# Kernel tuning notes

Hardware: AMD Instinct MI355X
Metric: run time of the kernel (lower is better)

Reference implementation:

```python
import jax, jax.numpy as jnp
import numpy as np

N, E, T = 50000, 800000, 3
FIN, H, D, FE = 256, 4, 64, 64
NEG_SLOPE = 0.2


def setup_inputs() -> dict:
    key = jax.random.key(0)
    ks = jax.random.split(key, 10)
    x = jax.random.normal(ks[0], (N, FIN), dtype=jnp.float32)
    edge_src = jax.random.randint(ks[1], (E,), 0, N, dtype=jnp.int32)
    edge_dst = jax.random.randint(ks[2], (E,), 0, N, dtype=jnp.int32)
    edge_type = jax.random.randint(ks[3], (E,), 0, T, dtype=jnp.int32)
    s = 1.0 / np.sqrt(FIN)
    W = jax.random.normal(ks[4], (FIN, H * D), dtype=jnp.float32) * s
    edge_emb = jax.random.normal(ks[5], (T, FE), dtype=jnp.float32)
    W_e = jax.random.normal(ks[6], (FE, H * FE), dtype=jnp.float32) * (1.0 / np.sqrt(FE))
    attn_l = jax.random.normal(ks[7], (H, D), dtype=jnp.float32) * (1.0 / np.sqrt(D))
    attn_r = jax.random.normal(ks[8], (H, D), dtype=jnp.float32) * (1.0 / np.sqrt(D))
    attn_e = jax.random.normal(ks[9], (H, FE), dtype=jnp.float32) * (1.0 / np.sqrt(FE))
    return {"x": x, "edge_src": edge_src, "edge_dst": edge_dst,
            "edge_type": edge_type, "W": W, "edge_emb": edge_emb,
            "W_e": W_e, "attn_l": attn_l, "attn_r": attn_r, "attn_e": attn_e}


def reference(x, edge_src, edge_dst, edge_type, W, edge_emb, W_e, attn_l, attn_r, attn_e):
    # node projection: [N, H, D]
    feat = (x @ W).reshape(N, H, D)
    # per-node, per-head attention scalars
    el = jnp.einsum('nhd,hd->nh', feat, attn_l)  # [N, H]
    er = jnp.einsum('nhd,hd->nh', feat, attn_r)  # [N, H]
    # per-edge-type attention scalar: edge_emb[t] @ W_e -> [T, H, FE]
    e_feat = (edge_emb @ W_e).reshape(T, H, FE)
    ee = jnp.einsum('the,he->th', e_feat, attn_e)  # [T, H]
    # per-edge logits, leaky-relu
    logits = jax.nn.leaky_relu(el[edge_src] + er[edge_dst] + ee[edge_type], NEG_SLOPE)  # [E, H]
    # edge softmax over incoming edges of each dst node (all etypes together)
    seg_max = jax.ops.segment_max(logits, edge_dst, num_segments=N)  # [N, H]
    seg_max = jnp.where(jnp.isfinite(seg_max), seg_max, 0.0)
    expl = jnp.exp(logits - seg_max[edge_dst])  # [E, H]
    seg_sum = jax.ops.segment_sum(expl, edge_dst, num_segments=N)  # [N, H]
    a = expl / seg_sum[edge_dst]  # [E, H]
    # weighted scatter-sum aggregation: sum over incoming edges
    msg = feat[edge_src] * a[:, :, None]  # [E, H, D]
    out = jax.ops.segment_sum(msg, edge_dst, num_segments=N)  # [N, H, D]
    return out, a
```

## Files before the change

kernel.cpp:

```cpp
#include <hip/hip_runtime.h>
#include <hip/hip_bf16.h>
#include <math.h>

#define N_NODES 50000
#define E_EDGES 800000
#define T_TYPES 3
#define MAXDEG 64
#define NEG_SLOPE 0.2f
#define GEMM_BLOCKS 391

typedef __attribute__((ext_vector_type(8))) short short8;
typedef __attribute__((ext_vector_type(4))) float f32x4;

__device__ inline short f2bf(float f) {
    __hip_bfloat16 h = __float2bfloat16(f);
    union { __hip_bfloat16 b; short s; } u;
    u.b = h;
    return u.s;
}
__device__ inline float bf2f(short s) {
    union { unsigned u; float f; } v;
    v.u = ((unsigned)(unsigned short)s) << 16;
    return v.f;
}

__global__ void k_prep(const float* __restrict__ W, short* __restrict__ Wt,
                       const float* __restrict__ edge_emb, const float* __restrict__ W_e,
                       const float* __restrict__ attn_e, float* __restrict__ ee,
                       unsigned* __restrict__ deg) {
    int b = blockIdx.x;
    if (b < 256) {
        int n = b, k = threadIdx.x;
        Wt[n * 256 + k] = f2bf(W[k * 256 + n]);
    } else if (b < 256 + T_TYPES) {
        int t = b - 256;
        int j = threadIdx.x;
        int h = j >> 6;
        float ae = attn_e[j];
        float v = 0.f;
        #pragma unroll
        for (int k = 0; k < 64; ++k) v += edge_emb[t * 64 + k] * W_e[k * 256 + j];
        v *= ae;
        #pragma unroll
        for (int o = 32; o; o >>= 1) v += __shfl_xor(v, o, 64);
        if ((j & 63) == 0) ee[t * 4 + h] = v;
    } else {
        int i = (b - 256 - T_TYPES) * 256 + threadIdx.x;
        if (i < N_NODES) deg[i] = 0u;
    }
}

__global__ __launch_bounds__(512) void k_gs(const float* __restrict__ x, const short* __restrict__ Wt,
                                            const float* __restrict__ attn_l, const float* __restrict__ attn_r,
                                            short* __restrict__ featb, float* __restrict__ el,
                                            float* __restrict__ er,
                                            const int* __restrict__ esrc, const int* __restrict__ edst,
                                            const int* __restrict__ etype, unsigned* __restrict__ deg,
                                            unsigned* __restrict__ A) {
    __shared__ short a_lds[2][128 * 40];
    if (blockIdx.x >= GEMM_BLOCKS) {
        int e = (blockIdx.x - GEMM_BLOCKS) * 512 + threadIdx.x;
        if (e < E_EDGES) {
            int s = esrc[e], d = edst[e], t = etype[e];
            unsigned rank = atomicAdd(&deg[d], 1u);
            if (rank < MAXDEG)
                A[d * MAXDEG + rank] = (unsigned)s | ((unsigned)t << 16);
        }
        return;
    }

    const int tid = threadIdx.x;
    const int wid = tid >> 6;
    const int lane = tid & 63;
    const int wr = wid >> 2;
    const int wc = wid & 3;
    const int l15 = lane & 15;
    const int lq = lane >> 4;
    const int m0 = blockIdx.x * 128;

    f32x4 acc[4][4];
    #pragma unroll
    for (int mf = 0; mf < 4; ++mf)
        #pragma unroll
        for (int nf = 0; nf < 4; ++nf)
            acc[mf][nf] = (f32x4){0.f, 0.f, 0.f, 0.f};

    const int sr = tid >> 2;
    const int sc = (tid & 3) * 8;
    int gm = m0 + sr;
    if (gm >= N_NODES) gm = N_NODES - 1;
    const float* xrow = &x[(size_t)gm * 256];

    {
        float4 v0 = *reinterpret_cast<const float4*>(&xrow[sc]);
        float4 v1 = *reinterpret_cast<const float4*>(&xrow[sc + 4]);
        short8 s;
        s[0] = f2bf(v0.x); s[1] = f2bf(v0.y); s[2] = f2bf(v0.z); s[3] = f2bf(v0.w);
        s[4] = f2bf(v1.x); s[5] = f2bf(v1.y); s[6] = f2bf(v1.z); s[7] = f2bf(v1.w);
        *reinterpret_cast<short8*>(&a_lds[0][sr * 40 + sc]) = s;
    }
    __syncthreads();

    #pragma unroll
    for (int k0 = 0; k0 < 256; k0 += 32) {
        const int cur = (k0 >> 5) & 1;
        const bool hasNext = (k0 + 32) < 256;
        float4 v0, v1;
        if (hasNext) {
            v0 = *reinterpret_cast<const float4*>(&xrow[k0 + 32 + sc]);
            v1 = *reinterpret_cast<const float4*>(&xrow[k0 + 32 + sc + 4]);
        }
        short8 av[4], bv[4];
        #pragma unroll
        for (int mf = 0; mf < 4; ++mf)
            av[mf] = *reinterpret_cast<const short8*>(&a_lds[cur][(wr * 64 + mf * 16 + l15) * 40 + lq * 8]);
        #pragma unroll
        for (int nf = 0; nf < 4; ++nf) {
            int n = wc * 64 + nf * 16 + l15;
            bv[nf] = *reinterpret_cast<const short8*>(&Wt[(size_t)n * 256 + k0 + lq * 8]);
        }
        if (hasNext) {
            short8 s;
            s[0] = f2bf(v0.x); s[1] = f2bf(v0.y); s[2] = f2bf(v0.z); s[3] = f2bf(v0.w);
            s[4] = f2bf(v1.x); s[5] = f2bf(v1.y); s[6] = f2bf(v1.z); s[7] = f2bf(v1.w);
            *reinterpret_cast<short8*>(&a_lds[cur ^ 1][sr * 40 + sc]) = s;
        }
        #pragma unroll
        for (int mf = 0; mf < 4; ++mf)
            #pragma unroll
            for (int nf = 0; nf < 4; ++nf)
                acc[mf][nf] = __builtin_amdgcn_mfma_f32_16x16x32_bf16(av[mf], bv[nf], acc[mf][nf], 0, 0, 0);
        __syncthreads();
    }

    float al[4], ar[4];
    #pragma unroll
    for (int nf = 0; nf < 4; ++nf) {
        al[nf] = attn_l[wc * 64 + nf * 16 + l15];
        ar[nf] = attn_r[wc * 64 + nf * 16 + l15];
    }
    #pragma unroll
    for (int mf = 0; mf < 4; ++mf) {
        #pragma unroll
        for (int i = 0; i < 4; ++i) {
            int m = m0 + wr * 64 + mf * 16 + lq * 4 + i;
            bool ok = m < N_NODES;
            float pl = 0.f, pr = 0.f;
            #pragma unroll
            for (int nf = 0; nf < 4; ++nf) {
                float v = acc[mf][nf][i];
                if (ok) featb[(size_t)m * 256 + wc * 64 + nf * 16 + l15] = f2bf(v);
                pl += v * al[nf];
                pr += v * ar[nf];
            }
            #pragma unroll
            for (int o = 1; o < 16; o <<= 1) {
                pl += __shfl_xor(pl, o, 64);
                pr += __shfl_xor(pr, o, 64);
            }
            if (ok && l15 == 0) {
                el[m * 4 + wc] = pl;
                er[m * 4 + wc] = pr;
            }
        }
    }
}

__global__ __launch_bounds__(256) void k_agg(const unsigned* __restrict__ deg, const unsigned* __restrict__ A,
                                             const float* __restrict__ el, const float* __restrict__ er,
                                             const float* __restrict__ ee, const short* __restrict__ featb,
                                             float* __restrict__ out, float* __restrict__ invp) {
    const int wave = threadIdx.x >> 6;
    const int lane = threadIdx.x & 63;
    const int n = blockIdx.x * 4 + wave;
    if (n >= N_NODES) return;
    const int half = lane >> 5;
    const int l32 = lane & 31;
    const int h = l32 >> 3;
    unsigned cnt = deg[n];
    if (cnt > MAXDEG) cnt = MAXDEG;
    const unsigned base = (unsigned)n * MAXDEG;

    const float ern = er[n * 4 + h];
    const float ee0 = ee[h], ee1 = ee[4 + h], ee2 = ee[8 + h];

    float s0 = 0.f, s1 = 0.f;
    float a0[8], a1[8];
    #pragma unroll
    for (int j = 0; j < 8; ++j) { a0[j] = 0.f; a1[j] = 0.f; }
    {
        unsigned i = half;
        for (; i + 2 < cnt; i += 4) {
            unsigned p0 = A[base + i];
            unsigned p1 = A[base + i + 2];
            unsigned src0 = p0 & 0xFFFFu, t0 = p0 >> 16;
            unsigned src1 = p1 & 0xFFFFu, t1 = p1 >> 16;
            float el0 = el[src0 * 4 + h];
            float el1 = el[src1 * 4 + h];
            short8 f0 = *reinterpret_cast<const short8*>(&featb[(size_t)src0 * 256 + l32 * 8]);
            short8 f1 = *reinterpret_cast<const short8*>(&featb[(size_t)src1 * 256 + l32 * 8]);
            float z0 = (el0 + ern) + (t0 == 0 ? ee0 : (t0 == 1 ? ee1 : ee2));
            float z1 = (el1 + ern) + (t1 == 0 ? ee0 : (t1 == 1 ? ee1 : ee2));
            z0 = z0 > 0.f ? z0 : NEG_SLOPE * z0;
            z1 = z1 > 0.f ? z1 : NEG_SLOPE * z1;
            float w0 = __expf(z0);
            float w1 = __expf(z1);
            s0 += w0; s1 += w1;
            #pragma unroll
            for (int j = 0; j < 8; ++j) {
                a0[j] += w0 * bf2f(f0[j]);
                a1[j] += w1 * bf2f(f1[j]);
            }
        }
        for (; i < cnt; i += 2) {
            unsigned p0 = A[base + i];
            unsigned src0 = p0 & 0xFFFFu, t0 = p0 >> 16;
            float el0 = el[src0 * 4 + h];
            short8 f0 = *reinterpret_cast<const short8*>(&featb[(size_t)src0 * 256 + l32 * 8]);
            float z0 = (el0 + ern) + (t0 == 0 ? ee0 : (t0 == 1 ? ee1 : ee2));
            z0 = z0 > 0.f ? z0 : NEG_SLOPE * z0;
            float w0 = __expf(z0);
            s0 += w0;
            #pragma unroll
            for (int j = 0; j < 8; ++j) a0[j] += w0 * bf2f(f0[j]);
        }
    }
    float s = s0 + s1;
    s += __shfl_xor(s, 32, 64);
    #pragma unroll
    for (int j = 0; j < 8; ++j) {
        a0[j] += a1[j];
        a0[j] += __shfl_xor(a0[j], 32, 64);
    }
    float inv = (cnt > 0) ? 1.f / s : 0.f;

    if (half == 0) {
        float4 o0, o1;
        o0.x = a0[0] * inv; o0.y = a0[1] * inv; o0.z = a0[2] * inv; o0.w = a0[3] * inv;
        o1.x = a0[4] * inv; o1.y = a0[5] * inv; o1.z = a0[6] * inv; o1.w = a0[7] * inv;
        *reinterpret_cast<float4*>(&out[(size_t)n * 256 + l32 * 8]) = o0;
        *reinterpret_cast<float4*>(&out[(size_t)n * 256 + l32 * 8 + 4]) = o1;
        if ((l32 & 7) == 0) invp[n * 4 + h] = inv;
    }
}

__global__ void k_edge(const int* __restrict__ esrc, const int* __restrict__ edst,
                       const int* __restrict__ etype, const float* __restrict__ el,
                       const float* __restrict__ er, const float* __restrict__ ee,
                       const float* __restrict__ invp, float* __restrict__ a_out) {
    int e = blockIdx.x * 256 + threadIdx.x;
    if (e >= E_EDGES) return;
    int s = esrc[e], d = edst[e], t = etype[e];
    float4 l = *reinterpret_cast<const float4*>(&el[s * 4]);
    float4 r = *reinterpret_cast<const float4*>(&er[d * 4]);
    float4 q = *reinterpret_cast<const float4*>(&ee[t * 4]);
    float4 iv = *reinterpret_cast<const float4*>(&invp[d * 4]);
    float4 z;
    z.x = (l.x + r.x) + q.x;
    z.y = (l.y + r.y) + q.y;
    z.z = (l.z + r.z) + q.z;
    z.w = (l.w + r.w) + q.w;
    z.x = z.x > 0.f ? z.x : NEG_SLOPE * z.x;
    z.y = z.y > 0.f ? z.y : NEG_SLOPE * z.y;
    z.z = z.z > 0.f ? z.z : NEG_SLOPE * z.z;
    z.w = z.w > 0.f ? z.w : NEG_SLOPE * z.w;
    float4 av;
    av.x = __expf(z.x) * iv.x;
    av.y = __expf(z.y) * iv.y;
    av.z = __expf(z.z) * iv.z;
    av.w = __expf(z.w) * iv.w;
    *reinterpret_cast<float4*>(&a_out[(size_t)e * 4]) = av;
}

extern "C" void kernel_launch(void* const* d_in, const int* in_sizes, int n_in,
                              void* d_out, int out_size, void* d_ws, size_t ws_size,
                              hipStream_t stream) {
    const float* x        = (const float*)d_in[0];
    const int*   edge_src = (const int*)d_in[1];
    const int*   edge_dst = (const int*)d_in[2];
    const int*   edge_type= (const int*)d_in[3];
    const float* W        = (const float*)d_in[4];
    const float* edge_emb = (const float*)d_in[5];
    const float* W_e      = (const float*)d_in[6];
    const float* attn_l   = (const float*)d_in[7];
    const float* attn_r   = (const float*)d_in[8];
    const float* attn_e   = (const float*)d_in[9];

    float* out   = (float*)d_out;
    float* a_out = (float*)d_out + (size_t)N_NODES * 256;

    char* ws = (char*)d_ws;
    short*    featb   = (short*)(ws + 0);
    float*    el      = (float*)(ws + 25600000);
    float*    er      = (float*)(ws + 26400000);
    float*    ee      = (float*)(ws + 27200000);
    unsigned* deg     = (unsigned*)(ws + 27200064);
    float*    invp    = (float*)(ws + 27400064);
    unsigned* A       = (unsigned*)(ws + 28200064);
    short*    Wt      = (short*)(ws + 41000064);

    const int degBlocks = (N_NODES + 255) / 256;
    k_prep<<<256 + T_TYPES + degBlocks, 256, 0, stream>>>(W, Wt, edge_emb, W_e, attn_e, ee, deg);

    const int scatterBlocks = (E_EDGES + 511) / 512;
    k_gs<<<GEMM_BLOCKS + scatterBlocks, 512, 0, stream>>>(x, Wt, attn_l, attn_r, featb, el, er,
                                                          edge_src, edge_dst, edge_type, deg, A);

    k_agg<<<(N_NODES + 3) / 4, 256, 0, stream>>>(deg, A, el, er, ee, featb, out, invp);
    k_edge<<<(E_EDGES + 255) / 256, 256, 0, stream>>>(edge_src, edge_dst, edge_type,
                                                      el, er, ee, invp, a_out);
}
```

Before: 150.9 us.

## Drop LDS staging in projection GEMM, load x fragments directly per wave

The fused GEMM+scatter kernel now uses 256-thread blocks covering 64 rows instead of 512-thread blocks covering 128 rows. Each wave reads its own x fragments straight from global memory, converts them to bf16 in registers, and feeds them to MFMA. This removes the shared-memory double buffer and the per-iteration barriers. The cost is that each of the four waves in a block re-reads the same x rows (4x redundant global/L2 traffic for x), and the x load pattern becomes strided per lane. Smaller blocks may also improve occupancy and overlap with the scatter blocks.

```diff
diff --git a/kernel.cpp b/kernel.cpp
--- a/kernel.cpp
+++ b/kernel.cpp
@@ -7,7 +7,7 @@
 #define T_TYPES 3
 #define MAXDEG 64
 #define NEG_SLOPE 0.2f
-#define GEMM_BLOCKS 391
+#define GEMM_BLOCKS 782
 
 typedef __attribute__((ext_vector_type(8))) short short8;
 typedef __attribute__((ext_vector_type(4))) float f32x4;
@@ -50,16 +50,15 @@
     }
 }
 
-__global__ __launch_bounds__(512) void k_gs(const float* __restrict__ x, const short* __restrict__ Wt,
+__global__ __launch_bounds__(256) void k_gs(const float* __restrict__ x, const short* __restrict__ Wt,
                                             const float* __restrict__ attn_l, const float* __restrict__ attn_r,
                                             short* __restrict__ featb, float* __restrict__ el,
                                             float* __restrict__ er,
                                             const int* __restrict__ esrc, const int* __restrict__ edst,
                                             const int* __restrict__ etype, unsigned* __restrict__ deg,
                                             unsigned* __restrict__ A) {
-    __shared__ short a_lds[2][128 * 40];
     if (blockIdx.x >= GEMM_BLOCKS) {
-        int e = (blockIdx.x - GEMM_BLOCKS) * 512 + threadIdx.x;
+        int e = (blockIdx.x - GEMM_BLOCKS) * 256 + threadIdx.x;
         if (e < E_EDGES) {
             int s = esrc[e], d = edst[e], t = etype[e];
             unsigned rank = atomicAdd(&deg[d], 1u);
@@ -70,13 +69,20 @@
     }
 
     const int tid = threadIdx.x;
-    const int wid = tid >> 6;
+    const int wc = tid >> 6;
     const int lane = tid & 63;
-    const int wr = wid >> 2;
-    const int wc = wid & 3;
     const int l15 = lane & 15;
     const int lq = lane >> 4;
-    const int m0 = blockIdx.x * 128;
+    const int m0 = blockIdx.x * 64;
+
+    const float* xr[4];
+    #pragma unroll
+    for (int mf = 0; mf < 4; ++mf) {
+        int r = m0 + mf * 16 + l15;
+        if (r >= N_NODES) r = N_NODES - 1;
+        xr[mf] = &x[(size_t)r * 256];
+    }
+    const short* wbase = &Wt[(size_t)(wc * 64 + l15) * 256 + lq * 8];
 
     f32x4 acc[4][4];
     #pragma unroll
@@ -85,52 +91,26 @@
         for (int nf = 0; nf < 4; ++nf)
             acc[mf][nf] = (f32x4){0.f, 0.f, 0.f, 0.f};
 
-    const int sr = tid >> 2;
-    const int sc = (tid & 3) * 8;
-    int gm = m0 + sr;
-    if (gm >= N_NODES) gm = N_NODES - 1;
-    const float* xrow = &x[(size_t)gm * 256];
-
-    {
-        float4 v0 = *reinterpret_cast<const float4*>(&xrow[sc]);
-        float4 v1 = *reinterpret_cast<const float4*>(&xrow[sc + 4]);
-        short8 s;
-        s[0] = f2bf(v0.x); s[1] = f2bf(v0.y); s[2] = f2bf(v0.z); s[3] = f2bf(v0.w);
-        s[4] = f2bf(v1.x); s[5] = f2bf(v1.y); s[6] = f2bf(v1.z); s[7] = f2bf(v1.w);
-        *reinterpret_cast<short8*>(&a_lds[0][sr * 40 + sc]) = s;
-    }
-    __syncthreads();
-
-    #pragma unroll
+    #pragma unroll 2
     for (int k0 = 0; k0 < 256; k0 += 32) {
-        const int cur = (k0 >> 5) & 1;
-        const bool hasNext = (k0 + 32) < 256;
-        float4 v0, v1;
-        if (hasNext) {
-            v0 = *reinterpret_cast<const float4*>(&xrow[k0 + 32 + sc]);
-            v1 = *reinterpret_cast<const float4*>(&xrow[k0 + 32 + sc + 4]);
-        }
         short8 av[4], bv[4];
         #pragma unroll
-        for (int mf = 0; mf < 4; ++mf)
-            av[mf] = *reinterpret_cast<const short8*>(&a_lds[cur][(wr * 64 + mf * 16 + l15) * 40 + lq * 8]);
-        #pragma unroll
-        for (int nf = 0; nf < 4; ++nf) {
-            int n = wc * 64 + nf * 16 + l15;
-            bv[nf] = *reinterpret_cast<const short8*>(&Wt[(size_t)n * 256 + k0 + lq * 8]);
-        }
-        if (hasNext) {
+        for (int mf = 0; mf < 4; ++mf) {
+            float4 u0 = *reinterpret_cast<const float4*>(&xr[mf][k0 + lq * 8]);
+            float4 u1 = *reinterpret_cast<const float4*>(&xr[mf][k0 + lq * 8 + 4]);
             short8 s;
-            s[0] = f2bf(v0.x); s[1] = f2bf(v0.y); s[2] = f2bf(v0.z); s[3] = f2bf(v0.w);
-            s[4] = f2bf(v1.x); s[5] = f2bf(v1.y); s[6] = f2bf(v1.z); s[7] = f2bf(v1.w);
-            *reinterpret_cast<short8*>(&a_lds[cur ^ 1][sr * 40 + sc]) = s;
-        }
+            s[0] = f2bf(u0.x); s[1] = f2bf(u0.y); s[2] = f2bf(u0.z); s[3] = f2bf(u0.w);
+            s[4] = f2bf(u1.x); s[5] = f2bf(u1.y); s[6] = f2bf(u1.z); s[7] = f2bf(u1.w);
+            av[mf] = s;
+        }
+        #pragma unroll
+        for (int nf = 0; nf < 4; ++nf)
+            bv[nf] = *reinterpret_cast<const short8*>(&wbase[nf * 16 * 256 + k0]);
         #pragma unroll
         for (int mf = 0; mf < 4; ++mf)
             #pragma unroll
             for (int nf = 0; nf < 4; ++nf)
                 acc[mf][nf] = __builtin_amdgcn_mfma_f32_16x16x32_bf16(av[mf], bv[nf], acc[mf][nf], 0, 0, 0);
-        __syncthreads();
     }
 
     float al[4], ar[4];
@@ -143,7 +123,7 @@
     for (int mf = 0; mf < 4; ++mf) {
         #pragma unroll
         for (int i = 0; i < 4; ++i) {
-            int m = m0 + wr * 64 + mf * 16 + lq * 4 + i;
+            int m = m0 + mf * 16 + lq * 4 + i;
             bool ok = m < N_NODES;
             float pl = 0.f, pr = 0.f;
             #pragma unroll
@@ -302,8 +282,8 @@
     const int degBlocks = (N_NODES + 255) / 256;
     k_prep<<<256 + T_TYPES + degBlocks, 256, 0, stream>>>(W, Wt, edge_emb, W_e, attn_e, ee, deg);
 
-    const int scatterBlocks = (E_EDGES + 511) / 512;
-    k_gs<<<GEMM_BLOCKS + scatterBlocks, 512, 0, stream>>>(x, Wt, attn_l, attn_r, featb, el, er,
+    const int scatterBlocks = (E_EDGES + 255) / 256;
+    k_gs<<<GEMM_BLOCKS + scatterBlocks, 256, 0, stream>>>(x, Wt, attn_l, attn_r, featb, el, er,
                                                           edge_src, edge_dst, edge_type, deg, A);
 
     k_agg<<<(N_NODES + 3) / 4, 256, 0, stream>>>(deg, A, el, er, ee, featb, out, invp);
```

After: 173.2 us. 1.15x slower.
